# Kernel optimization log

Measured on AMD Instinct MI355X. Metric: run time of the kernel, lower is better.

## Reference

```python
import jax, jax.numpy as jnp
import numpy as np

# S4D diagonal SSM kernel generation (disc='zoh', real_type='exp', no state, rate=1.0)
H = 768      # model width (number of SSM copies)
N = 64       # state size per SSM
CH = 1       # kernel channels
NSSM = 768   # n_ssm == H -> repeat = 1 (untied)
L_VAL = 2048 # target kernel length


def setup_inputs() -> dict:
    key = jax.random.key(0)
    k_dt, k_C = jax.random.split(key, 2)
    # dt log-uniform in [1e-3, 1e-1]
    log_dt = np.log(1e-3) + jax.random.uniform(k_dt, (H,), dtype=jnp.float32) * (np.log(1e-1) - np.log(1e-3))
    # B = 1 + 0j  (standard S4D init), stored as real/imag pair
    B_ri = jnp.concatenate([jnp.ones((NSSM, N, 1), jnp.float32), jnp.zeros((NSSM, N, 1), jnp.float32)], axis=-1)
    # A = -0.5 + i*pi*n  (S4D-Lin); real_type='exp' -> inv_A_real = log(-A_real) = log(0.5)
    inv_A_real = jnp.full((NSSM, N), np.log(0.5), dtype=jnp.float32)
    A_imag = jnp.tile(np.pi * jnp.arange(N, dtype=jnp.float32)[None, :], (NSSM, 1))
    C_ri = jax.random.normal(k_C, (CH, H, N, 2), dtype=jnp.float32)
    return {"log_dt": log_dt, "B_ri": B_ri, "inv_A_real": inv_A_real,
            "A_imag": A_imag, "C_ri": C_ri, "L": L_VAL}


def reference(log_dt, B_ri, inv_A_real, A_imag, C_ri, L):
    dt = jnp.exp(log_dt)                               # (H,)
    A = -jnp.exp(inv_A_real) + 1j * A_imag             # (n_ssm, N) complex
    rep = H // A.shape[0]
    A = jnp.tile(A, (rep, 1))                          # (H, N)
    B = B_ri[..., 0] + 1j * B_ri[..., 1]               # (n_ssm, N)
    B = jnp.tile(B, (rep, 1))[None]                    # (1, H, N)
    C = C_ri[..., 0] + 1j * C_ri[..., 1]               # (CH, H, N)
    C = (B[:, None, :, :] * C).reshape(-1, H, N)       # (CH, H, N)
    dtA = A * dt[:, None]                              # (H, N)
    # ZOH discretization of C
    C = C * (jnp.exp(dtA) - 1.0) / A                   # (CH, H, N)
    # log-Vandermonde: K[c,h,l] = 2*Re( sum_n C[c,h,n] * exp(dtA[h,n] * l) )
    ell = jnp.arange(L, dtype=jnp.float32)
    V = jnp.exp(dtA[:, :, None] * ell)                 # (H, N, L) complex64 -- dominant intermediate
    K = 2.0 * jnp.einsum('chn,hnl->chl', C, V).real    # (CH, H, L)
    return K.astype(jnp.float32)
```

## Files before the change

### kernel.cpp

```cpp
#include <hip/hip_runtime.h>
#include <math.h>


typedef float v2f __attribute__((ext_vector_type(2)));

#define H_DIM 768
#define N_DIM 64
#define L_DIM 2048
#define TPB   256
#define LTH   64
#define LCH   32

__global__ __launch_bounds__(TPB, 3) void s4d_gen_kernel(
    const float* __restrict__ log_dt,
    const float* __restrict__ B_ri,
    const float* __restrict__ inv_A_real,
    const float* __restrict__ A_imag,
    const float* __restrict__ C_ri,
    float* __restrict__ out)
{
    __shared__ float4 sP0[N_DIM];
    __shared__ float4 sP1[N_DIM];
    __shared__ v2f    sRedV[3][LCH][LTH];

    const int h  = blockIdx.x;
    const int t  = threadIdx.x;
    const int nb = t >> 6;
    const int tl = t & 63;

    if (t < N_DIM) {
        const int n   = t;
        const int idx = h * N_DIM + n;
        const float dt = expf(log_dt[h]);
        const float Ar = -expf(inv_A_real[idx]);
        const float Ai = A_imag[idx];
        const float dtAr = Ar * dt;
        const float dtAi = Ai * dt;
        const float e  = expf(dtAr);
        float s, c;
        sincosf(dtAi, &s, &c);
        const float wr = e * c, wi = e * s;
        const float inv = 1.0f / (Ar * Ar + Ai * Ai);
        const float nr = wr - 1.0f, ni = wi;
        const float qr = (nr * Ar + ni * Ai) * inv;
        const float qi = (ni * Ar - nr * Ai) * inv;
        const float Br = B_ri[2 * idx], Bi = B_ri[2 * idx + 1];
        const float Cr = C_ri[2 * idx], Ci = C_ri[2 * idx + 1];
        const float BCr = Br * Cr - Bi * Ci;
        const float BCi = Br * Ci + Bi * Cr;
        const float Gr = 2.0f * (BCr * qr - BCi * qi);
        const float Gi = 2.0f * (BCr * qi + BCi * qr);
        const double revs32 = (double)dtAi * (32.0 / (2.0 * M_PI));
        const float  r32f   = (float)(revs32 - floor(revs32));
        const float  l2m32  = dtAr * (32.0f * 1.4426950408889634f);
        sP0[n] = make_float4(r32f, l2m32, Gr, Gi);
        sP1[n] = make_float4(Gr * wr - Gi * wi, Gr * wi + Gi * wr,
                             2.0f * wr, -(wr * wr + wi * wi));
    }
    __syncthreads();

    v2f acc2[LCH];
    #pragma unroll
    for (int j = 0; j < LCH; ++j) acc2[j] = (v2f){0.0f, 0.0f};

    const int   nbase = nb * 16;
    const float tlf   = (float)tl;

    #pragma unroll
    for (int half = 0; half < 2; ++half) {
        const int n0 = nbase + half * 8;

        float s0s[8], s1s[8], c1s[8], nc2s[8];
        #pragma unroll
        for (int k = 0; k < 8; ++k) {
            const float4 p = sP0[n0 + k];
            const float4 q = sP1[n0 + k];
            const float f  = __builtin_amdgcn_fractf(p.x * tlf);
            const float m  = __builtin_amdgcn_exp2f(p.y * tlf);
            const float cs = __builtin_amdgcn_cosf(f);
            const float sn = __builtin_amdgcn_sinf(f);
            const float ur = m * cs, ui = m * sn;
            s0s[k]  = fmaf(p.z, ur, -(p.w * ui));
            s1s[k]  = fmaf(q.x, ur, -(q.y * ui));
            c1s[k]  = q.z;
            nc2s[k] = q.w;
        }
        v2f S0[4], S1[4], C1[4], NC2[4];
        #pragma unroll
        for (int k = 0; k < 4; ++k) {
            S0[k]  = (v2f){s0s[2*k],  s0s[2*k+1]};
            S1[k]  = (v2f){s1s[2*k],  s1s[2*k+1]};
            C1[k]  = (v2f){c1s[2*k],  c1s[2*k+1]};
            NC2[k] = (v2f){nc2s[2*k], nc2s[2*k+1]};
        }

        #pragma unroll
        for (int j = 0; j < LCH; ++j) {
            const v2f t1 = S0[0] + S0[1];
            const v2f t2 = S0[2] + S0[3];
            acc2[j] += t1;
            acc2[j] += t2;
            #pragma unroll
            for (int k = 0; k < 4; ++k) {
                v2f tt = C1[k] * S1[k];
                v2f nn = __builtin_elementwise_fma(NC2[k], S0[k], tt);
                S0[k] = S1[k]; S1[k] = nn;
            }
        }
    }

    if (nb != 0) {
        #pragma unroll
        for (int j = 0; j < LCH; ++j) sRedV[nb - 1][j][tl] = acc2[j];
    }
    __syncthreads();
    if (nb == 0) {
        #pragma unroll
        for (int j = 0; j < LCH; ++j) {
            const v2f a = sRedV[0][j][tl];
            const v2f b = sRedV[1][j][tl];
            const v2f c = sRedV[2][j][tl];
            acc2[j] += a + b + c;
        }
        float acc[LCH];
        #pragma unroll
        for (int j = 0; j < LCH; ++j) acc[j] = acc2[j].x + acc2[j].y;
        float* op = out + (size_t)h * L_DIM + tl * LCH;
        #pragma unroll
        for (int j = 0; j < LCH; j += 4) {
            *reinterpret_cast<float4*>(op + j) =
                make_float4(acc[j], acc[j + 1], acc[j + 2], acc[j + 3]);
        }
    }
}

extern "C" void kernel_launch(void* const* d_in, const int* in_sizes, int n_in,
                              void* d_out, int out_size, void* d_ws, size_t ws_size,
                              hipStream_t stream) {
    const float* log_dt     = (const float*)d_in[0];
    const float* B_ri       = (const float*)d_in[1];
    const float* inv_A_real = (const float*)d_in[2];
    const float* A_imag     = (const float*)d_in[3];
    const float* C_ri       = (const float*)d_in[4];
    float* out = (float*)d_out;
    hipLaunchKernelGGL(s4d_gen_kernel, dim3(H_DIM), dim3(TPB), 0, stream,
                       log_dt, B_ri, inv_A_real, A_imag, C_ri, out);
}
```

Before: 73.74 us.

## Split each SSM row across two blocks with shorter recurrence chunks

Each row's output length is now split between two blocks, and each thread handles 16 output positions instead of 32. This doubles the grid size and halves the accumulator registers per thread, and the launch-bounds target rises to allow more resident blocks for latency hiding. The final shared-memory reduction becomes a two-step tree. In exchange, the per-row parameter setup is computed twice and more direct exp/sincos evaluations are needed to seed the recurrences.

```diff
diff --git a/kernel.cpp b/kernel.cpp
--- a/kernel.cpp
+++ b/kernel.cpp
@@ -9,9 +9,9 @@
 #define L_DIM 2048
 #define TPB   256
 #define LTH   64
-#define LCH   32
+#define LCH   16
 
-__global__ __launch_bounds__(TPB, 3) void s4d_gen_kernel(
+__global__ __launch_bounds__(TPB, 6) void s4d_gen_kernel(
     const float* __restrict__ log_dt,
     const float* __restrict__ B_ri,
     const float* __restrict__ inv_A_real,
@@ -21,12 +21,13 @@
 {
     __shared__ float4 sP0[N_DIM];
     __shared__ float4 sP1[N_DIM];
-    __shared__ v2f    sRedV[3][LCH][LTH];
+    __shared__ v2f    sRedV[2][LCH][LTH];
 
-    const int h  = blockIdx.x;
-    const int t  = threadIdx.x;
-    const int nb = t >> 6;
-    const int tl = t & 63;
+    const int h    = blockIdx.x >> 1;
+    const int half = blockIdx.x & 1;
+    const int t    = threadIdx.x;
+    const int nb   = t >> 6;
+    const int tl   = t & 63;
 
     if (t < N_DIM) {
         const int n   = t;
@@ -50,10 +51,10 @@
         const float BCi = Br * Ci + Bi * Cr;
         const float Gr = 2.0f * (BCr * qr - BCi * qi);
         const float Gi = 2.0f * (BCr * qi + BCi * qr);
-        const double revs32 = (double)dtAi * (32.0 / (2.0 * M_PI));
-        const float  r32f   = (float)(revs32 - floor(revs32));
-        const float  l2m32  = dtAr * (32.0f * 1.4426950408889634f);
-        sP0[n] = make_float4(r32f, l2m32, Gr, Gi);
+        const double revs16 = (double)dtAi * (16.0 / (2.0 * M_PI));
+        const float  r16f   = (float)(revs16 - floor(revs16));
+        const float  l2m16  = dtAr * (16.0f * 1.4426950408889634f);
+        sP0[n] = make_float4(r16f, l2m16, Gr, Gi);
         sP1[n] = make_float4(Gr * wr - Gi * wi, Gr * wi + Gi * wr,
                              2.0f * wr, -(wr * wr + wi * wi));
     }
@@ -64,34 +65,31 @@
     for (int j = 0; j < LCH; ++j) acc2[j] = (v2f){0.0f, 0.0f};
 
     const int   nbase = nb * 16;
-    const float tlf   = (float)tl;
+    const float ef    = (float)(half * 64 + tl);
 
     #pragma unroll
-    for (int half = 0; half < 2; ++half) {
-        const int n0 = nbase + half * 8;
+    for (int hf = 0; hf < 2; ++hf) {
+        const int n0 = nbase + hf * 8;
 
-        float s0s[8], s1s[8], c1s[8], nc2s[8];
-        #pragma unroll
-        for (int k = 0; k < 8; ++k) {
-            const float4 p = sP0[n0 + k];
-            const float4 q = sP1[n0 + k];
-            const float f  = __builtin_amdgcn_fractf(p.x * tlf);
-            const float m  = __builtin_amdgcn_exp2f(p.y * tlf);
-            const float cs = __builtin_amdgcn_cosf(f);
-            const float sn = __builtin_amdgcn_sinf(f);
-            const float ur = m * cs, ui = m * sn;
-            s0s[k]  = fmaf(p.z, ur, -(p.w * ui));
-            s1s[k]  = fmaf(q.x, ur, -(q.y * ui));
-            c1s[k]  = q.z;
-            nc2s[k] = q.w;
-        }
         v2f S0[4], S1[4], C1[4], NC2[4];
         #pragma unroll
-        for (int k = 0; k < 4; ++k) {
-            S0[k]  = (v2f){s0s[2*k],  s0s[2*k+1]};
-            S1[k]  = (v2f){s1s[2*k],  s1s[2*k+1]};
-            C1[k]  = (v2f){c1s[2*k],  c1s[2*k+1]};
-            NC2[k] = (v2f){nc2s[2*k], nc2s[2*k+1]};
+        for (int p = 0; p < 4; ++p) {
+            const float4 pa = sP0[n0 + 2 * p],     pb = sP0[n0 + 2 * p + 1];
+            const float4 qa = sP1[n0 + 2 * p],     qb = sP1[n0 + 2 * p + 1];
+            const float fa = __builtin_amdgcn_fractf(pa.x * ef);
+            const float fb = __builtin_amdgcn_fractf(pb.x * ef);
+            const float ma = __builtin_amdgcn_exp2f(pa.y * ef);
+            const float mb = __builtin_amdgcn_exp2f(pb.y * ef);
+            const float ca = __builtin_amdgcn_cosf(fa), sa = __builtin_amdgcn_sinf(fa);
+            const float cb = __builtin_amdgcn_cosf(fb), sb = __builtin_amdgcn_sinf(fb);
+            const float ura = ma * ca, uia = ma * sa;
+            const float urb = mb * cb, uib = mb * sb;
+            S0[p]  = (v2f){fmaf(pa.z, ura, -(pa.w * uia)),
+                           fmaf(pb.z, urb, -(pb.w * uib))};
+            S1[p]  = (v2f){fmaf(qa.x, ura, -(qa.y * uia)),
+                           fmaf(qb.x, urb, -(qb.y * uib))};
+            C1[p]  = (v2f){qa.z, qb.z};
+            NC2[p] = (v2f){qa.w, qb.w};
         }
 
         #pragma unroll
@@ -109,23 +107,28 @@
         }
     }
 
-    if (nb != 0) {
+    if (nb >= 2) {
         #pragma unroll
-        for (int j = 0; j < LCH; ++j) sRedV[nb - 1][j][tl] = acc2[j];
+        for (int j = 0; j < LCH; ++j) sRedV[nb - 2][j][tl] = acc2[j];
+    }
+    __syncthreads();
+    if (nb < 2) {
+        #pragma unroll
+        for (int j = 0; j < LCH; ++j) acc2[j] += sRedV[nb][j][tl];
+    }
+    __syncthreads();
+    if (nb == 1) {
+        #pragma unroll
+        for (int j = 0; j < LCH; ++j) sRedV[0][j][tl] = acc2[j];
     }
     __syncthreads();
     if (nb == 0) {
         #pragma unroll
-        for (int j = 0; j < LCH; ++j) {
-            const v2f a = sRedV[0][j][tl];
-            const v2f b = sRedV[1][j][tl];
-            const v2f c = sRedV[2][j][tl];
-            acc2[j] += a + b + c;
-        }
+        for (int j = 0; j < LCH; ++j) acc2[j] += sRedV[0][j][tl];
         float acc[LCH];
         #pragma unroll
         for (int j = 0; j < LCH; ++j) acc[j] = acc2[j].x + acc2[j].y;
-        float* op = out + (size_t)h * L_DIM + tl * LCH;
+        float* op = out + (size_t)h * L_DIM + half * (L_DIM / 2) + tl * LCH;
         #pragma unroll
         for (int j = 0; j < LCH; j += 4) {
             *reinterpret_cast<float4*>(op + j) =
@@ -143,6 +146,6 @@
     const float* A_imag     = (const float*)d_in[3];
     const float* C_ri       = (const float*)d_in[4];
     float* out = (float*)d_out;
-    hipLaunchKernelGGL(s4d_gen_kernel, dim3(H_DIM), dim3(TPB), 0, stream,
+    hipLaunchKernelGGL(s4d_gen_kernel, dim3(H_DIM * 2), dim3(TPB), 0, stream,
                        log_dt, B_ri, inv_A_real, A_imag, C_ri, out);
 }
```

After: 74.40 us. About the same (+0.9%).
